# Optimization experiments

Hardware: AMD Instinct MI355X
Metric: run time of the kernel (lower is better)

The kernel has to match this reference:

```python
import jax, jax.numpy as jnp
import numpy as np

DIM = 1024


def setup_inputs() -> dict:
    key = jax.random.key(0)
    ks = jax.random.split(key, 10)
    B, S, D = 4, 2048, DIM
    std = 1.0 / np.sqrt(D)  # torch Linear default uniform bound
    return {
        "query": jax.random.normal(ks[0], (B, S, D), jnp.float32),
        "key": jax.random.normal(ks[1], (B, S, D), jnp.float32),
        "value": jax.random.normal(ks[2], (B, S, D), jnp.float32),
        "context": jnp.zeros((D,), jnp.float32),
        "Wq": jax.random.uniform(ks[3], (D, D), jnp.float32, -std, std),
        "bq": jax.random.uniform(ks[4], (D,), jnp.float32, -std, std),
        "Wk": jax.random.uniform(ks[5], (D, D), jnp.float32, -std, std),
        "bk": jax.random.uniform(ks[6], (D,), jnp.float32, -std, std),
        "Wv": jax.random.uniform(ks[7], (D, D), jnp.float32, -std, std),
        "bv": jax.random.uniform(ks[8], (D,), jnp.float32, -std, std),
    }


def reference(query, key, value, context, Wq, bq, Wk, bk, Wv, bv):
    scale = query.shape[-1] ** -0.5
    # torch Linear: x @ W.T + b
    q = (query + context) @ Wq.T + bq          # [B,S,D]
    k = (key + context) @ Wk.T + bk            # [B,S,D]
    v = value @ Wv.T + bv                      # [B,S,D]
    scores = jnp.einsum("bqd,bkd->bqk", q, k) * scale  # [B,S,S]
    weights = jax.nn.softmax(scores, axis=-1)
    return jnp.einsum("bqk,bkd->bqd", weights, v)
```

## Files before the change

### kernel.cpp

```cpp
#include <hip/hip_runtime.h>

typedef __attribute__((ext_vector_type(8))) short bf16x8;
typedef __attribute__((ext_vector_type(4))) float floatx4;

constexpr int BATCH = 4;
constexpr int SEQ   = 2048;
constexpr int DIMN  = 1024;
constexpr int M1    = BATCH * SEQ;

constexpr int BM = 128, BN = 128, BK = 32;

__device__ __forceinline__ short f2bf(float f) {
    union { float f; unsigned u; } x; x.f = f;
    unsigned r = x.u + 0x7fffu + ((x.u >> 16) & 1u);
    return (short)(r >> 16);
}
__device__ __forceinline__ float bf2f(short s) {
    union { unsigned u; float f; } x; x.u = ((unsigned)(unsigned short)s) << 16;
    return x.f;
}

__device__ __forceinline__ void async16(const void* g, void* l) {
    __builtin_amdgcn_global_load_lds(
        (const __attribute__((address_space(1))) unsigned int*)g,
        (__attribute__((address_space(3))) unsigned int*)l, 16, 0, 0);
}

template<bool OUT_BF16>
__device__ __forceinline__ void gemm_core(
    const short* __restrict__ Ab, int lda,
    const short* __restrict__ Bb, int ldb,
    void* __restrict__ Cb, int ldc,
    const float* __restrict__ bias, int K, float scale,
    int m0, int n0)
{
    __shared__ short As[2][BM][BK];
    __shared__ short Bs[2][BN][BK];

    const int tid  = threadIdx.x;
    const int lane = tid & 63;
    const int wave = tid >> 6;
    const int wr = wave >> 1, wc = wave & 1;
    const int lr = lane & 15;
    const int lq = lane >> 4;

    floatx4 acc[4][4];
    #pragma unroll
    for (int i = 0; i < 4; ++i)
        #pragma unroll
        for (int j = 0; j < 4; ++j) acc[i][j] = (floatx4)(0.f);

    auto stage = [&](int k0, int bi) {
        #pragma unroll
        for (int h = 0; h < 2; ++h) {
            const int c   = tid + h * 256;
            const int row = c >> 2;
            const int kc  = (c & 3) * 8;
            async16(Ab + (size_t)(m0 + row) * lda + k0 + kc, &As[bi][row][kc]);
            async16(Bb + (size_t)(n0 + row) * ldb + k0 + kc, &Bs[bi][row][kc]);
        }
    };

    const int NK = K / BK;
    stage(0, 0);
    __syncthreads();

    for (int it = 0; it < NK; ++it) {
        const int bi = it & 1;
        if (it + 1 < NK) stage((it + 1) * BK, bi ^ 1);

        bf16x8 af[4], bfr[4];
        #pragma unroll
        for (int i = 0; i < 4; ++i)
            af[i] = *(const bf16x8*)&As[bi][wr * 64 + i * 16 + lr][lq * 8];
        #pragma unroll
        for (int j = 0; j < 4; ++j)
            bfr[j] = *(const bf16x8*)&Bs[bi][wc * 64 + j * 16 + lr][lq * 8];
        #pragma unroll
        for (int i = 0; i < 4; ++i)
            #pragma unroll
            for (int j = 0; j < 4; ++j)
                acc[i][j] = __builtin_amdgcn_mfma_f32_16x16x32_bf16(
                    af[i], bfr[j], acc[i][j], 0, 0, 0);

        if (it + 1 < NK) __syncthreads();
    }

    #pragma unroll
    for (int j = 0; j < 4; ++j) {
        const int gn = n0 + wc * 64 + j * 16 + lr;
        const float bv = bias ? bias[gn] : 0.f;
        #pragma unroll
        for (int i = 0; i < 4; ++i) {
            #pragma unroll
            for (int r = 0; r < 4; ++r) {
                const int gm = m0 + wr * 64 + i * 16 + lq * 4 + r;
                const float v = acc[i][j][r] * scale + bv;
                if (OUT_BF16) {
                    ((short*)Cb)[(size_t)gm * ldc + gn] = f2bf(v);
                } else {
                    ((float*)Cb)[(size_t)gm * ldc + gn] = v;
                }
            }
        }
    }
}

__global__ __launch_bounds__(256)
void proj_qk(const short* __restrict__ xq, const short* __restrict__ xk,
             const short* __restrict__ Wq_, const short* __restrict__ Wk_,
             const float* __restrict__ bq_, const float* __restrict__ bk_,
             short* __restrict__ q, short* __restrict__ k)
{
    const int b   = blockIdx.x;
    const int xcd = b & 7;
    const int i   = b >> 3;
    const int z   = i >> 6;
    const int mm  = (i >> 3) & 7;
    const int nn  = i & 7;
    gemm_core<true>(z ? xk : xq, DIMN, z ? Wk_ : Wq_, DIMN,
                    z ? (void*)k : (void*)q, DIMN,
                    z ? bk_ : bq_, DIMN, 1.f,
                    (xcd * 8 + mm) * BM, nn * BN);
}

__global__ __launch_bounds__(256)
void proj_v(const short* __restrict__ xv, const short* __restrict__ Wv_,
            const float* __restrict__ bv_, short* __restrict__ vp)
{
    const int b   = blockIdx.x;
    const int xcd = b & 7;
    const int i   = b >> 3;
    const int mm  = i >> 3;
    const int nn  = i & 7;
    gemm_core<true>(xv, DIMN, Wv_, DIMN, (void*)vp, DIMN, bv_, DIMN, 1.f,
                    (xcd * 8 + mm) * BM, nn * BN);
}

__global__ __launch_bounds__(256)
void gemm_scores(const short* __restrict__ q, const short* __restrict__ k,
                 short* __restrict__ S, float scale)
{
    const int b   = blockIdx.x;
    const int xcd = b & 7;
    const int i   = b >> 3;
    const int bz  = xcd >> 1;
    const int mh  = xcd & 1;
    const int mm  = i >> 4;
    const int nn  = i & 15;
    gemm_core<true>(q + (size_t)bz * SEQ * DIMN, DIMN,
                    k + (size_t)bz * SEQ * DIMN, DIMN,
                    (void*)(S + (size_t)bz * SEQ * SEQ), SEQ,
                    nullptr, DIMN, scale,
                    (mh * 8 + mm) * BM, nn * BN);
}

__global__ __launch_bounds__(256)
void gemm_pv(const short* __restrict__ P, const short* __restrict__ vt,
             float* __restrict__ O)
{
    const int b   = blockIdx.x;
    const int xcd = b & 7;
    const int i   = b >> 3;
    const int bz  = xcd >> 1;
    const int mh  = xcd & 1;
    const int mm  = i >> 3;
    const int nn  = i & 7;
    gemm_core<false>(P  + (size_t)bz * SEQ * SEQ,  SEQ,
                     vt + (size_t)bz * DIMN * SEQ, SEQ,
                     (void*)(O + (size_t)bz * SEQ * DIMN), DIMN,
                     nullptr, SEQ, 1.f,
                     (mh * 8 + mm) * BM, nn * BN);
}

__global__ __launch_bounds__(256)
void cvt_tri(const float* __restrict__ in0, short* __restrict__ out0,
             const float* __restrict__ in1, short* __restrict__ out1,
             const float* __restrict__ in2, short* __restrict__ out2, int n8)
{
    const int z = blockIdx.z;
    const float* in = (z == 0) ? in0 : (z == 1) ? in1 : in2;
    short* out      = (z == 0) ? out0 : (z == 1) ? out1 : out2;
    const int i = blockIdx.x * 256 + threadIdx.x;
    if (i >= n8) return;
    const float4 a0 = ((const float4*)in)[(size_t)i * 2];
    const float4 a1 = ((const float4*)in)[(size_t)i * 2 + 1];
    const float v[8] = {a0.x, a0.y, a0.z, a0.w, a1.x, a1.y, a1.z, a1.w};
    bf16x8 o;
    #pragma unroll
    for (int j = 0; j < 8; ++j) o[j] = f2bf(v[j]);
    *(bf16x8*)(out + (size_t)i * 8) = o;
}

__global__ __launch_bounds__(256)
void bias3(const float* __restrict__ Wq, const float* __restrict__ Wk,
           const float* __restrict__ Wv,
           const float* __restrict__ bq, const float* __restrict__ bk,
           const float* __restrict__ bv,
           const float* __restrict__ ctx,
           float* __restrict__ oq, float* __restrict__ ok, float* __restrict__ ov)
{
    const int z = blockIdx.y;
    const float* W = (z == 0) ? Wq : (z == 1) ? Wk : Wv;
    const float* b = (z == 0) ? bq : (z == 1) ? bk : bv;
    float*       o = (z == 0) ? oq : (z == 1) ? ok : ov;
    const int n    = blockIdx.x * 4 + (threadIdx.x >> 6);
    const int lane = threadIdx.x & 63;
    float s = 0.f;
    if (z < 2) {
        const float* row = W + (size_t)n * DIMN;
        for (int k = lane * 4; k < DIMN; k += 256) {
            const float4 x = *(const float4*)(row + k);
            const float4 c = *(const float4*)(ctx + k);
            s += x.x * c.x + x.y * c.y + x.z * c.z + x.w * c.w;
        }
        #pragma unroll
        for (int off = 32; off > 0; off >>= 1) s += __shfl_xor(s, off);
    }
    if (lane == 0) o[n] = b[n] + s;
}

__global__ __launch_bounds__(256)
void transpose_v(const short* __restrict__ in, short* __restrict__ out)
{
    __shared__ short t[64][68];
    const int b  = blockIdx.z;
    const int d0 = blockIdx.x * 64;
    const int s0 = blockIdx.y * 64;
    const int r  = threadIdx.x >> 3;
    const int c  = (threadIdx.x & 7) * 8;
    #pragma unroll
    for (int h = 0; h < 2; ++h) {
        const int s = r + h * 32;
        bf16x8 v = *(const bf16x8*)(in + ((size_t)b * SEQ + s0 + s) * DIMN + d0 + c);
        #pragma unroll
        for (int j = 0; j < 8; ++j) t[c + j][s] = v[j];
    }
    __syncthreads();
    #pragma unroll
    for (int h = 0; h < 2; ++h) {
        const int d = r + h * 32;
        bf16x8 v;
        #pragma unroll
        for (int j = 0; j < 8; ++j) v[j] = t[d][c + j];
        *(bf16x8*)(out + ((size_t)b * DIMN + d0 + d) * SEQ + s0 + c) = v;
    }
}

__global__ __launch_bounds__(256)
void softmax_kernel(short* __restrict__ P)
{
    const int row  = blockIdx.x;
    short* p = P + (size_t)row * SEQ;
    const int t    = threadIdx.x;
    const int lane = t & 63;
    const int wave = t >> 6;
    __shared__ float red[8];

    bf16x8 raw = *(const bf16x8*)(p + t * 8);
    float v[8];
    float mx = -1e30f;
    #pragma unroll
    for (int j = 0; j < 8; ++j) { v[j] = bf2f(raw[j]); mx = fmaxf(mx, v[j]); }
    #pragma unroll
    for (int off = 32; off > 0; off >>= 1) mx = fmaxf(mx, __shfl_xor(mx, off));
    if (lane == 0) red[wave] = mx;
    __syncthreads();
    mx = fmaxf(fmaxf(red[0], red[1]), fmaxf(red[2], red[3]));

    float e[8], s = 0.f;
    #pragma unroll
    for (int j = 0; j < 8; ++j) { e[j] = __expf(v[j] - mx); s += e[j]; }
    #pragma unroll
    for (int off = 32; off > 0; off >>= 1) s += __shfl_xor(s, off);
    if (lane == 0) red[4 + wave] = s;
    __syncthreads();
    s = red[4] + red[5] + red[6] + red[7];
    const float inv = 1.f / s;

    bf16x8 o;
    #pragma unroll
    for (int j = 0; j < 8; ++j) o[j] = f2bf(e[j] * inv);
    *(bf16x8*)(p + t * 8) = o;
}

extern "C" void kernel_launch(void* const* d_in, const int* in_sizes, int n_in,
                              void* d_out, int out_size, void* d_ws, size_t ws_size,
                              hipStream_t stream)
{
    const float* query = (const float*)d_in[0];
    const float* key_  = (const float*)d_in[1];
    const float* value = (const float*)d_in[2];
    const float* ctx   = (const float*)d_in[3];
    const float* Wq    = (const float*)d_in[4];
    const float* bq    = (const float*)d_in[5];
    const float* Wk    = (const float*)d_in[6];
    const float* bk    = (const float*)d_in[7];
    const float* Wv    = (const float*)d_in[8];
    const float* bv    = (const float*)d_in[9];

    char* ws = (char*)d_ws;
    const size_t MB = 1ull << 20;
    short* xq   = (short*)(ws);
    short* xk   = (short*)(ws + 16 * MB);
    short* q_b  = (short*)(ws + 32 * MB);
    short* k_b  = (short*)(ws + 48 * MB);
    short* Wq_b = (short*)(ws + 64 * MB);
    short* Wk_b = (short*)(ws + 66 * MB);
    short* Wv_b = (short*)(ws + 68 * MB);
    float* bq_e = (float*)(ws + 70 * MB);
    float* bk_e = (float*)(ws + 70 * MB + 4096);
    float* bv_e = (float*)(ws + 70 * MB + 8192);
    short* xv   = (short*)(ws);
    short* vp   = (short*)(ws + 16 * MB);
    short* S_b  = (short*)(ws);
    short* v_t  = (short*)(ws + 64 * MB);

    dim3 blk(256);
    const int W8 = DIMN * DIMN / 8;
    const int X8 = M1 * DIMN / 8;

    cvt_tri<<<dim3(W8 / 256, 1, 3), blk, 0, stream>>>(Wq, Wq_b, Wk, Wk_b, Wv, Wv_b, W8);
    bias3<<<dim3(DIMN / 4, 3), blk, 0, stream>>>(Wq, Wk, Wv, bq, bk, bv, ctx,
                                                 bq_e, bk_e, bv_e);

    cvt_tri<<<dim3(X8 / 256, 1, 2), blk, 0, stream>>>(query, xq, key_, xk,
                                                      nullptr, nullptr, X8);
    proj_qk<<<dim3(1024), blk, 0, stream>>>(xq, xk, Wq_b, Wk_b, bq_e, bk_e, q_b, k_b);

    cvt_tri<<<dim3(X8 / 256, 1, 1), blk, 0, stream>>>(value, xv, nullptr, nullptr,
                                                      nullptr, nullptr, X8);
    proj_v<<<dim3(512), blk, 0, stream>>>(xv, Wv_b, bv_e, vp);
    transpose_v<<<dim3(DIMN / 64, SEQ / 64, BATCH), blk, 0, stream>>>(vp, v_t);

    const float scale = 1.0f / 32.0f;
    gemm_scores<<<dim3(1024), blk, 0, stream>>>(q_b, k_b, S_b, scale);

    softmax_kernel<<<dim3(M1), blk, 0, stream>>>(S_b);

    gemm_pv<<<dim3(512), blk, 0, stream>>>(S_b, v_t, (float*)d_out);
}
```

Measured before the change: 374.1 us.

## Merge QKV projections, use 128x64 tiles for PV, reorder softmax rows by XCD

Fuses the Q/K and V projections into a single 1536-block launch, with all three input conversions done in one cvt launch. The V staging buffers move into the output buffer so they do not alias the Q/K workspace. The GEMM core is templated on N-tile width, and the PV GEMM uses 128x64 tiles so it launches 1024 blocks instead of 512, improving occupancy across CUs. Staging uses precomputed incrementing pointers, and softmax rows are remapped so each XCD works on a contiguous region of S; the cost is lower per-block reuse of the B tile in PV.

```diff
diff --git a/kernel.cpp b/kernel.cpp
--- a/kernel.cpp
+++ b/kernel.cpp
@@ -8,7 +8,7 @@
 constexpr int DIMN  = 1024;
 constexpr int M1    = BATCH * SEQ;
 
-constexpr int BM = 128, BN = 128, BK = 32;
+constexpr int BM = 128, BK = 32;
 
 __device__ __forceinline__ short f2bf(float f) {
     union { float f; unsigned u; } x; x.f = f;
@@ -26,7 +26,7 @@
         (__attribute__((address_space(3))) unsigned int*)l, 16, 0, 0);
 }
 
-template<bool OUT_BF16>
+template<bool OUT_BF16, int WJ>
 __device__ __forceinline__ void gemm_core(
     const short* __restrict__ Ab, int lda,
     const short* __restrict__ Bb, int ldb,
@@ -34,8 +34,9 @@
     const float* __restrict__ bias, int K, float scale,
     int m0, int n0)
 {
+    constexpr int BN_ = WJ * 32;
     __shared__ short As[2][BM][BK];
-    __shared__ short Bs[2][BN][BK];
+    __shared__ short Bs[2][BN_][BK];
 
     const int tid  = threadIdx.x;
     const int lane = tid & 63;
@@ -44,42 +45,46 @@
     const int lr = lane & 15;
     const int lq = lane >> 4;
 
-    floatx4 acc[4][4];
+    const int row = tid >> 2;
+    const int kc  = (tid & 3) * 8;
+    const short* pA = Ab + (size_t)(m0 + row) * lda + kc;
+    const short* pB = Bb + (size_t)(n0 + row) * ldb + kc;
+    const size_t stA = (size_t)64 * lda;
+    const size_t stB = (size_t)64 * ldb;
+
+    floatx4 acc[4][WJ];
     #pragma unroll
     for (int i = 0; i < 4; ++i)
         #pragma unroll
-        for (int j = 0; j < 4; ++j) acc[i][j] = (floatx4)(0.f);
-
-    auto stage = [&](int k0, int bi) {
-        #pragma unroll
-        for (int h = 0; h < 2; ++h) {
-            const int c   = tid + h * 256;
-            const int row = c >> 2;
-            const int kc  = (c & 3) * 8;
-            async16(Ab + (size_t)(m0 + row) * lda + k0 + kc, &As[bi][row][kc]);
-            async16(Bb + (size_t)(n0 + row) * ldb + k0 + kc, &Bs[bi][row][kc]);
-        }
+        for (int j = 0; j < WJ; ++j) acc[i][j] = (floatx4)(0.f);
+
+    auto stage = [&](int bi) {
+        async16(pA,       &As[bi][row][kc]);
+        async16(pA + stA, &As[bi][row + 64][kc]);
+        async16(pB,       &Bs[bi][row][kc]);
+        if (WJ == 4) async16(pB + stB, &Bs[bi][row + 64][kc]);
+        pA += BK; pB += BK;
     };
 
     const int NK = K / BK;
-    stage(0, 0);
+    stage(0);
     __syncthreads();
 
     for (int it = 0; it < NK; ++it) {
         const int bi = it & 1;
-        if (it + 1 < NK) stage((it + 1) * BK, bi ^ 1);
-
-        bf16x8 af[4], bfr[4];
+        if (it + 1 < NK) stage(bi ^ 1);
+
+        bf16x8 af[4], bfr[WJ];
         #pragma unroll
         for (int i = 0; i < 4; ++i)
             af[i] = *(const bf16x8*)&As[bi][wr * 64 + i * 16 + lr][lq * 8];
         #pragma unroll
-        for (int j = 0; j < 4; ++j)
-            bfr[j] = *(const bf16x8*)&Bs[bi][wc * 64 + j * 16 + lr][lq * 8];
+        for (int j = 0; j < WJ; ++j)
+            bfr[j] = *(const bf16x8*)&Bs[bi][wc * (16 * WJ) + j * 16 + lr][lq * 8];
         #pragma unroll
         for (int i = 0; i < 4; ++i)
             #pragma unroll
-            for (int j = 0; j < 4; ++j)
+            for (int j = 0; j < WJ; ++j)
                 acc[i][j] = __builtin_amdgcn_mfma_f32_16x16x32_bf16(
                     af[i], bfr[j], acc[i][j], 0, 0, 0);
 
@@ -87,8 +92,8 @@
     }
 
     #pragma unroll
-    for (int j = 0; j < 4; ++j) {
-        const int gn = n0 + wc * 64 + j * 16 + lr;
+    for (int j = 0; j < WJ; ++j) {
+        const int gn = n0 + wc * (16 * WJ) + j * 16 + lr;
         const float bv = bias ? bias[gn] : 0.f;
         #pragma unroll
         for (int i = 0; i < 4; ++i) {
@@ -107,10 +112,13 @@
 }
 
 __global__ __launch_bounds__(256)
-void proj_qk(const short* __restrict__ xq, const short* __restrict__ xk,
-             const short* __restrict__ Wq_, const short* __restrict__ Wk_,
-             const float* __restrict__ bq_, const float* __restrict__ bk_,
-             short* __restrict__ q, short* __restrict__ k)
+void proj_qkv(const short* __restrict__ xq, const short* __restrict__ xk,
+              const short* __restrict__ xv,
+              const short* __restrict__ Wq_, const short* __restrict__ Wk_,
+              const short* __restrict__ Wv_,
+              const float* __restrict__ bq_, const float* __restrict__ bk_,
+              const float* __restrict__ bv_,
+              short* __restrict__ q, short* __restrict__ k, short* __restrict__ vp)
 {
     const int b   = blockIdx.x;
     const int xcd = b & 7;
@@ -118,23 +126,12 @@
     const int z   = i >> 6;
     const int mm  = (i >> 3) & 7;
     const int nn  = i & 7;
-    gemm_core<true>(z ? xk : xq, DIMN, z ? Wk_ : Wq_, DIMN,
-                    z ? (void*)k : (void*)q, DIMN,
-                    z ? bk_ : bq_, DIMN, 1.f,
-                    (xcd * 8 + mm) * BM, nn * BN);
-}
-
-__global__ __launch_bounds__(256)
-void proj_v(const short* __restrict__ xv, const short* __restrict__ Wv_,
-            const float* __restrict__ bv_, short* __restrict__ vp)
-{
-    const int b   = blockIdx.x;
-    const int xcd = b & 7;
-    const int i   = b >> 3;
-    const int mm  = i >> 3;
-    const int nn  = i & 7;
-    gemm_core<true>(xv, DIMN, Wv_, DIMN, (void*)vp, DIMN, bv_, DIMN, 1.f,
-                    (xcd * 8 + mm) * BM, nn * BN);
+    const short* X = (z == 0) ? xq : (z == 1) ? xk : xv;
+    const short* W = (z == 0) ? Wq_ : (z == 1) ? Wk_ : Wv_;
+    const float* bb = (z == 0) ? bq_ : (z == 1) ? bk_ : bv_;
+    short* O = (z == 0) ? q : (z == 1) ? k : vp;
+    gemm_core<true, 4>(X, DIMN, W, DIMN, (void*)O, DIMN, bb, DIMN, 1.f,
+                       (xcd * 8 + mm) * BM, nn * 128);
 }
 
 __global__ __launch_bounds__(256)
@@ -148,11 +145,11 @@
     const int mh  = xcd & 1;
     const int mm  = i >> 4;
     const int nn  = i & 15;
-    gemm_core<true>(q + (size_t)bz * SEQ * DIMN, DIMN,
-                    k + (size_t)bz * SEQ * DIMN, DIMN,
-                    (void*)(S + (size_t)bz * SEQ * SEQ), SEQ,
-                    nullptr, DIMN, scale,
-                    (mh * 8 + mm) * BM, nn * BN);
+    gemm_core<true, 4>(q + (size_t)bz * SEQ * DIMN, DIMN,
+                       k + (size_t)bz * SEQ * DIMN, DIMN,
+                       (void*)(S + (size_t)bz * SEQ * SEQ), SEQ,
+                       nullptr, DIMN, scale,
+                       (mh * 8 + mm) * BM, nn * 128);
 }
 
 __global__ __launch_bounds__(256)
@@ -164,13 +161,13 @@
     const int i   = b >> 3;
     const int bz  = xcd >> 1;
     const int mh  = xcd & 1;
-    const int mm  = i >> 3;
-    const int nn  = i & 7;
-    gemm_core<false>(P  + (size_t)bz * SEQ * SEQ,  SEQ,
-                     vt + (size_t)bz * DIMN * SEQ, SEQ,
-                     (void*)(O + (size_t)bz * SEQ * DIMN), DIMN,
-                     nullptr, SEQ, 1.f,
-                     (mh * 8 + mm) * BM, nn * BN);
+    const int mm  = i >> 4;
+    const int nn  = i & 15;
+    gemm_core<false, 2>(P  + (size_t)bz * SEQ * SEQ,  SEQ,
+                        vt + (size_t)bz * DIMN * SEQ, SEQ,
+                        (void*)(O + (size_t)bz * SEQ * DIMN), DIMN,
+                        nullptr, SEQ, 1.f,
+                        (mh * 8 + mm) * BM, nn * 64);
 }
 
 __global__ __launch_bounds__(256)
@@ -250,7 +247,10 @@
 __global__ __launch_bounds__(256)
 void softmax_kernel(short* __restrict__ P)
 {
-    const int row  = blockIdx.x;
+    const int bid = blockIdx.x;
+    const int xcd = bid & 7;
+    const int i   = bid >> 3;
+    const int row = (xcd >> 1) * SEQ + (xcd & 1) * 1024 + i;
     short* p = P + (size_t)row * SEQ;
     const int t    = threadIdx.x;
     const int lane = t & 63;
@@ -300,6 +300,7 @@
     const float* bv    = (const float*)d_in[9];
 
     char* ws = (char*)d_ws;
+    char* od = (char*)d_out;
     const size_t MB = 1ull << 20;
     short* xq   = (short*)(ws);
     short* xk   = (short*)(ws + 16 * MB);
@@ -311,10 +312,10 @@
     float* bq_e = (float*)(ws + 70 * MB);
     float* bk_e = (float*)(ws + 70 * MB + 4096);
     float* bv_e = (float*)(ws + 70 * MB + 8192);
-    short* xv   = (short*)(ws);
-    short* vp   = (short*)(ws + 16 * MB);
     short* S_b  = (short*)(ws);
     short* v_t  = (short*)(ws + 64 * MB);
+    short* xv   = (short*)(od);
+    short* vp   = (short*)(od + 16 * MB);
 
     dim3 blk(256);
     const int W8 = DIMN * DIMN / 8;
@@ -323,14 +324,10 @@
     cvt_tri<<<dim3(W8 / 256, 1, 3), blk, 0, stream>>>(Wq, Wq_b, Wk, Wk_b, Wv, Wv_b, W8);
     bias3<<<dim3(DIMN / 4, 3), blk, 0, stream>>>(Wq, Wk, Wv, bq, bk, bv, ctx,
                                                  bq_e, bk_e, bv_e);
-
-    cvt_tri<<<dim3(X8 / 256, 1, 2), blk, 0, stream>>>(query, xq, key_, xk,
-                                                      nullptr, nullptr, X8);
-    proj_qk<<<dim3(1024), blk, 0, stream>>>(xq, xk, Wq_b, Wk_b, bq_e, bk_e, q_b, k_b);
-
-    cvt_tri<<<dim3(X8 / 256, 1, 1), blk, 0, stream>>>(value, xv, nullptr, nullptr,
-                                                      nullptr, nullptr, X8);
-    proj_v<<<dim3(512), blk, 0, stream>>>(xv, Wv_b, bv_e, vp);
+    cvt_tri<<<dim3(X8 / 256, 1, 3), blk, 0, stream>>>(query, xq, key_, xk, value, xv, X8);
+
+    proj_qkv<<<dim3(1536), blk, 0, stream>>>(xq, xk, xv, Wq_b, Wk_b, Wv_b,
+                                             bq_e, bk_e, bv_e, q_b, k_b, vp);
     transpose_v<<<dim3(DIMN / 64, SEQ / 64, BATCH), blk, 0, stream>>>(vp, v_t);
 
     const float scale = 1.0f / 32.0f;
@@ -338,5 +335,5 @@
 
     softmax_kernel<<<dim3(M1), blk, 0, stream>>>(S_b);
 
-    gemm_pv<<<dim3(512), blk, 0, stream>>>(S_b, v_t, (float*)d_out);
-}
+    gemm_pv<<<dim3(1024), blk, 0, stream>>>(S_b, v_t, (float*)d_out);
+}
```

Measured after the change: 348.1 us. -7.0%, faster.
